# Optimization experiments

Hardware: AMD Instinct MI355X
Metric: run time of the kernel (lower is better)

The kernel has to match this reference:

```python
import jax, jax.numpy as jnp
import numpy as np

N = 50000       # nodes
E = 800000      # edges (before self-loops)
F_IN = 128      # in_channels
HID = 32        # hidden_channels per head
HEADS = 4
OUT = 16        # out_channels
NEG_SLOPE = 0.2 # PyG GATConv leaky_relu slope
EPS = 1e-16     # PyG softmax denominator eps
BN_EPS = 1e-5


def setup_inputs() -> dict:
    key = jax.random.key(0)
    ks = jax.random.split(key, 20)
    rn = lambda k, shp, s=0.1: (jax.random.normal(k, shp, jnp.float32) * s)
    x = jax.random.normal(ks[0], (N, F_IN), jnp.float32)
    edge_index = jax.random.randint(ks[1], (2, E), 0, N, dtype=jnp.int32)
    D0 = HEADS * HID  # 128
    return {
        "x": x, "edge_index": edge_index,
        # layer 0: GATConv(F_IN -> HID, heads=HEADS, concat=True)
        "W0": rn(ks[2], (F_IN, HEADS * HID)), "as0": rn(ks[3], (HEADS, HID)),
        "ad0": rn(ks[4], (HEADS, HID)), "b0": jnp.zeros((D0,), jnp.float32),
        "g0": jnp.ones((D0,), jnp.float32) + rn(ks[5], (D0,), 0.05),
        "be0": rn(ks[6], (D0,), 0.05),
        # layer 1: GATConv(D0 -> HID, heads=HEADS, concat=True)
        "W1": rn(ks[7], (D0, HEADS * HID)), "as1": rn(ks[8], (HEADS, HID)),
        "ad1": rn(ks[9], (HEADS, HID)), "b1": jnp.zeros((D0,), jnp.float32),
        "g1": jnp.ones((D0,), jnp.float32) + rn(ks[10], (D0,), 0.05),
        "be1": rn(ks[11], (D0,), 0.05),
        # layer 2: GATConv(D0 -> OUT, heads=1, concat=False)
        "W2": rn(ks[12], (D0, OUT)), "as2": rn(ks[13], (1, OUT)),
        "ad2": rn(ks[14], (1, OUT)), "b2": jnp.zeros((OUT,), jnp.float32),
    }


def _gat(x, src, dst, W, a_s, a_d, b, heads, ch, concat):
    n = x.shape[0]
    h = (x @ W).reshape(n, heads, ch)                       # [N,H,C]
    score_s = (h * a_s).sum(-1)                             # [N,H]
    score_d = (h * a_d).sum(-1)                             # [N,H]
    e = jax.nn.leaky_relu(score_s[src] + score_d[dst], NEG_SLOPE)  # [E,H]
    emax = jax.ops.segment_max(e, dst, num_segments=n)
    emax = jnp.where(jnp.isfinite(emax), emax, 0.0)
    p = jnp.exp(e - emax[dst])
    denom = jax.ops.segment_sum(p, dst, num_segments=n)
    alpha = p / (denom[dst] + EPS)                          # segment softmax over dst
    out = jax.ops.segment_sum(h[src] * alpha[:, :, None], dst, num_segments=n)
    out = out.reshape(n, heads * ch) if concat else out.mean(axis=1)
    return out + b


def _bn(x, g, be):
    m = x.mean(0)
    v = x.var(0)
    return (x - m) * jax.lax.rsqrt(v + BN_EPS) * g + be


def reference(x, edge_index, W0, as0, ad0, b0, g0, be0,
              W1, as1, ad1, b1, g1, be1, W2, as2, ad2, b2):
    n = x.shape[0]
    loop = jnp.arange(n, dtype=edge_index.dtype)
    src = jnp.concatenate([edge_index[0], loop])  # PyG add_self_loops
    dst = jnp.concatenate([edge_index[1], loop])
    h = _gat(x, src, dst, W0, as0, ad0, b0, HEADS, HID, True)
    h = jax.nn.elu(_bn(h, g0, be0))                 # dropout disabled (eval)
    h = _gat(h, src, dst, W1, as1, ad1, b1, HEADS, HID, True)
    h = jax.nn.elu(_bn(h, g1, be1))
    return _gat(h, src, dst, W2, as2, ad2, b2, 1, OUT, False)
```

## Files before the change

kernel.cpp:

```cpp
#include <hip/hip_runtime.h>
#include <hip/hip_bf16.h>
#include <math.h>

#define NEG_SLOPE 0.2f
#define EPS_SM 1e-16f
#define BN_EPS 1e-5f
#define RANK_BLOCKS 1024

typedef __attribute__((ext_vector_type(8))) short bf16x8;
typedef __attribute__((ext_vector_type(4))) float f32x4;

__device__ __forceinline__ float lrelu(float x) { return x > 0.f ? x : NEG_SLOPE * x; }
__device__ __forceinline__ ushort f2bf(float f) {
    uint u = __float_as_uint(f);
    return (ushort)((u + 0x7FFFu + ((u >> 16) & 1u)) >> 16);
}
__device__ __forceinline__ float bfl(uint u) { return __uint_as_float(u << 16); }
__device__ __forceinline__ float bfh(uint u) { return __uint_as_float(u & 0xFFFF0000u); }

__global__ void pack_w(const float* __restrict__ W0, const float* __restrict__ W1,
                       const float* __restrict__ W2, ushort* __restrict__ P0,
                       ushort* __restrict__ P1, ushort* __restrict__ P2) {
    int i = blockIdx.x * blockDim.x + threadIdx.x;
    const float* W;
    ushort* P;
    int NC, s;
    if (i < 16384) { W = W0; P = P0; NC = 128; s = i; }
    else if (i < 32768) { W = W1; P = P1; NC = 128; s = i - 16384; }
    else if (i < 34816) { W = W2; P = P2; NC = 16; s = i - 32768; }
    else return;
    int k = s / NC, col = s % NC;
    int CT = NC >> 4;
    int dst = (((k >> 5) * CT + (col >> 4)) << 9) +
              (((col & 15) | (((k >> 3) & 3) << 4)) << 3) + (k & 7);
    P[dst] = f2bf(W[s]);
}

template <int NC, int HEADS, bool XBN, bool RANKFUSE>
__global__ __launch_bounds__(256) void gemm_mfma(
    const void* __restrict__ Xv, const ushort* __restrict__ Wp, ushort* __restrict__ Hb,
    int n, const float* __restrict__ sumsP, const float* __restrict__ g,
    const float* __restrict__ be, const float* __restrict__ as_, const float* __restrict__ ad_,
    float* __restrict__ ss, float* __restrict__ sd,
    const int* __restrict__ dstE, int E, int* __restrict__ degP, ushort* __restrict__ rank) {
    int tid = threadIdx.x;
    if constexpr (RANKFUSE) {
        if ((int)blockIdx.x < RANK_BLOCKS) {
            const int T = RANK_BLOCKS * 256;
            int i = (int)blockIdx.x * 256 + tid;
            for (; i + 3 * T < E; i += 4 * T) {
                int d0 = dstE[i], d1 = dstE[i + T], d2 = dstE[i + 2 * T], d3 = dstE[i + 3 * T];
                ushort r0 = (ushort)atomicAdd(&degP[d0 << 4], 1);
                ushort r1 = (ushort)atomicAdd(&degP[d1 << 4], 1);
                ushort r2 = (ushort)atomicAdd(&degP[d2 << 4], 1);
                ushort r3 = (ushort)atomicAdd(&degP[d3 << 4], 1);
                rank[i] = r0;
                rank[i + T] = r1;
                rank[i + 2 * T] = r2;
                rank[i + 3 * T] = r3;
            }
            for (; i < E; i += T) rank[i] = (ushort)atomicAdd(&degP[dstE[i] << 4], 1);
            return;
        }
    }
    constexpr int CT = NC / 16;
    constexpr int FPH = NC / HEADS / 16;
    __shared__ __align__(16) ushort Xb[64 * 128];
    __shared__ float ssl[64 * HEADS], sdl[64 * HEADS];
    int bid = RANKFUSE ? ((int)blockIdx.x - RANK_BLOCKS) : (int)blockIdx.x;
    int row0 = bid * 64;
    if constexpr (!XBN) {
        const float* X = (const float*)Xv;
#pragma unroll
        for (int i = 0; i < 8; ++i) {
            int idx = tid + i * 256;
            int row = idx >> 5, q = idx & 31;
            int gr = row0 + row;
            float4 v = make_float4(0.f, 0.f, 0.f, 0.f);
            if (gr < n) v = ((const float4*)(X + (long)gr * 128))[q];
            ushort4 p = make_ushort4(f2bf(v.x), f2bf(v.y), f2bf(v.z), f2bf(v.w));
            int s = (q >> 1) ^ (row & 15);
            *(ushort4*)&Xb[row * 128 + s * 8 + (q & 1) * 4] = p;
        }
    } else {
        const ushort* X = (const ushort*)Xv;
        int c8 = (tid & 15) * 8;
        float inv_n = 1.f / (float)n;
        float bm[8], bs[8], bb[8];
#pragma unroll
        for (int j = 0; j < 8; ++j) {
            int ch = c8 + j;
            float m = sumsP[ch * 16] * inv_n;
            float vv = fmaxf(sumsP[(128 + ch) * 16] * inv_n - m * m, 0.f);
            bm[j] = m;
            bs[j] = rsqrtf(vv + BN_EPS) * g[ch];
            bb[j] = be[ch];
        }
#pragma unroll
        for (int i = 0; i < 4; ++i) {
            int idx = tid + i * 256;
            int row = idx >> 4, g8 = idx & 15;
            int gr = row0 + row;
            uint4 v = make_uint4(0, 0, 0, 0);
            if (gr < n) v = ((const uint4*)(X + (long)gr * 128))[g8];
            float a, b;
#define BNE(comp, j0)                                                  \
    a = bfl(comp); b = bfh(comp);                                      \
    a = (a - bm[j0]) * bs[j0] + bb[j0]; a = a > 0.f ? a : expm1f(a);   \
    b = (b - bm[j0 + 1]) * bs[j0 + 1] + bb[j0 + 1];                    \
    b = b > 0.f ? b : expm1f(b);                                       \
    comp = (uint)f2bf(a) | ((uint)f2bf(b) << 16);
            BNE(v.x, 0) BNE(v.y, 2) BNE(v.z, 4) BNE(v.w, 6)
#undef BNE
            int s = g8 ^ (row & 15);
            *(uint4*)&Xb[row * 128 + s * 8] = v;
        }
    }
    __syncthreads();
    int lane = tid & 63;
    int w = tid >> 6;
    int r0 = w * 16;
    int lrow = lane & 15, lhi = lane >> 4;
    f32x4 zero = {0.f, 0.f, 0.f, 0.f};
    f32x4 acc[CT];
#pragma unroll
    for (int f = 0; f < CT; ++f) acc[f] = zero;
    const ushort* xr = &Xb[(r0 + lrow) * 128];
#pragma unroll
    for (int ks = 0; ks < 4; ++ks) {
        int kg = ks * 4 + lhi;
        bf16x8 a = *(const bf16x8*)&xr[(kg ^ lrow) << 3];
#pragma unroll
        for (int f = 0; f < CT; ++f) {
            bf16x8 b = *(const bf16x8*)&Wp[((ks * CT + f) * 64 + lane) * 8];
            acc[f] = __builtin_amdgcn_mfma_f32_16x16x32_bf16(a, b, acc[f], 0, 0, 0);
        }
    }
    __syncthreads();
#pragma unroll
    for (int f = 0; f < CT; ++f)
#pragma unroll
        for (int j = 0; j < 4; ++j)
            Xb[(r0 + lhi * 4 + j) * NC + f * 16 + lrow] = f2bf(acc[f][j]);
    float asv[CT], adv[CT];
#pragma unroll
    for (int f = 0; f < CT; ++f) {
        asv[f] = as_[f * 16 + lrow];
        adv[f] = ad_[f * 16 + lrow];
    }
#pragma unroll
    for (int h = 0; h < HEADS; ++h) {
        float ps[4] = {}, pd[4] = {};
#pragma unroll
        for (int fi = 0; fi < FPH; ++fi) {
            int f = h * FPH + fi;
#pragma unroll
            for (int j = 0; j < 4; ++j) {
                ps[j] = fmaf(acc[f][j], asv[f], ps[j]);
                pd[j] = fmaf(acc[f][j], adv[f], pd[j]);
            }
        }
#pragma unroll
        for (int j = 0; j < 4; ++j) {
#pragma unroll
            for (int d = 1; d < 16; d <<= 1) {
                ps[j] += __shfl_xor(ps[j], d, 64);
                pd[j] += __shfl_xor(pd[j], d, 64);
            }
            if (lrow == 0) {
                ssl[(r0 + lhi * 4 + j) * HEADS + h] = ps[j];
                sdl[(r0 + lhi * 4 + j) * HEADS + h] = pd[j];
            }
        }
    }
    __syncthreads();
    constexpr int NU = 64 * NC / 8;
#pragma unroll
    for (int i = 0; i < (NU + 255) / 256; ++i) {
        int idx = tid + i * 256;
        if (idx < NU) {
            int row = idx / (NC / 8), c8i = idx % (NC / 8);
            int gr = row0 + row;
            if (gr < n) ((uint4*)&Hb[(long)gr * NC])[c8i] = ((const uint4*)Xb)[idx];
        }
    }
    if (tid < 64 * HEADS) {
        int row = tid / HEADS, hh = tid % HEADS;
        int gr = row0 + row;
        if (gr < n) {
            ss[(long)gr * HEADS + hh] = ssl[tid];
            sd[(long)gr * HEADS + hh] = sdl[tid];
        }
    }
}

__global__ void compact_deg(const int* __restrict__ degP, int* __restrict__ deg, int n) {
    int i = blockIdx.x * blockDim.x + threadIdx.x;
    if (i < n) deg[i] = degP[i << 4];
}

__global__ __launch_bounds__(1024) void scan_kernel(const int* __restrict__ deg,
                                                    int* __restrict__ offs, int n) {
    __shared__ int wsum[16];
    __shared__ int wpre[16];
    __shared__ int carry_s;
    int tid = threadIdx.x;
    int lane = tid & 63;
    int w = tid >> 6;
    if (tid == 0) carry_s = 0;
    __syncthreads();
    int nv = (n + 3) >> 2;
    for (int base = 0; base < nv; base += 1024) {
        int carry = carry_s;
        int gi = base + tid;
        int e0 = gi * 4;
        int4 v = make_int4(0, 0, 0, 0);
        if (e0 + 3 < n) {
            v = ((const int4*)deg)[gi];
        } else if (e0 < n) {
            v.x = deg[e0];
            if (e0 + 1 < n) v.y = deg[e0 + 1];
            if (e0 + 2 < n) v.z = deg[e0 + 2];
        }
        int tsum = v.x + v.y + v.z + v.w;
        int incl = tsum;
#pragma unroll
        for (int d = 1; d < 64; d <<= 1) {
            int t = __shfl_up(incl, d, 64);
            if (lane >= d) incl += t;
        }
        if (lane == 63) wsum[w] = incl;
        __syncthreads();
        if (w == 0 && lane < 16) {
            int s = wsum[lane];
#pragma unroll
            for (int d = 1; d < 16; d <<= 1) {
                int t = __shfl_up(s, d, 64);
                if (lane >= d) s += t;
            }
            wpre[lane] = s;
        }
        __syncthreads();
        int wbase = (w == 0) ? 0 : wpre[w - 1];
        int ex = carry + wbase + incl - tsum;
        if (e0 < n) {
            int4 o;
            o.x = ex;
            o.y = ex + v.x;
            o.z = o.y + v.y;
            o.w = o.z + v.z;
            if (e0 + 3 < n) {
                ((int4*)offs)[gi] = o;
            } else {
                offs[e0] = o.x;
                if (e0 + 1 < n) offs[e0 + 1] = o.y;
                if (e0 + 2 < n) offs[e0 + 2] = o.z;
            }
        }
        __syncthreads();
        if (tid == 1023) carry_s = carry + wpre[15];
        __syncthreads();
    }
    if (tid == 0) offs[n] = carry_s;
}

__global__ void scatter_kernel(const int* __restrict__ src, const int* __restrict__ dst,
                               const ushort* __restrict__ rank, const int* __restrict__ offs,
                               int E, int* __restrict__ srcs) {
    const int T = gridDim.x * blockDim.x;
    int i = blockIdx.x * blockDim.x + threadIdx.x;
    for (; i + 3 * T < E; i += 4 * T) {
        int d0 = dst[i], d1 = dst[i + T], d2 = dst[i + 2 * T], d3 = dst[i + 3 * T];
        int p0 = offs[d0] + (int)rank[i];
        int p1 = offs[d1] + (int)rank[i + T];
        int p2 = offs[d2] + (int)rank[i + 2 * T];
        int p3 = offs[d3] + (int)rank[i + 3 * T];
        srcs[p0] = src[i];
        srcs[p1] = src[i + T];
        srcs[p2] = src[i + 2 * T];
        srcs[p3] = src[i + 3 * T];
    }
    for (; i < E; i += T) srcs[offs[dst[i]] + (int)rank[i]] = src[i];
}

__global__ __launch_bounds__(256) void gat_gather4(
    const uint* __restrict__ hb, const float* __restrict__ ss, const float* __restrict__ sd,
    const int* __restrict__ offs, const int* __restrict__ srcs,
    const float* __restrict__ bias, ushort* __restrict__ outb, int n) {
    int wid = threadIdx.x >> 6;
    int lane = threadIdx.x & 63;
    int node = blockIdx.x * 4 + wid;
    if (node >= n) return;
    int off = offs[node];
    int dg = offs[node + 1] - off;
    int grp = lane >> 4;
    int ll = lane & 15;
    int hd = ll >> 2;
    float sdn = sd[node * 4 + hd];
    float es = lrelu(ss[node * 4 + hd] + sdn);
    const uint* hrow = hb + ll * 4;
    float acc[8] = {};
    float sm = 0.f;
    int i = grp;
    for (; i + 4 < dg; i += 8) {
        int s0 = srcs[off + i];
        int s1 = srcs[off + i + 4];
        float w0 = __expf(lrelu(ss[s0 * 4 + hd] + sdn));
        float w1 = __expf(lrelu(ss[s1 * 4 + hd] + sdn));
        uint4 h0 = *(const uint4*)(hrow + (long)s0 * 64);
        uint4 h1 = *(const uint4*)(hrow + (long)s1 * 64);
        sm += w0 + w1;
        acc[0] = fmaf(w0, bfl(h0.x), acc[0]); acc[0] = fmaf(w1, bfl(h1.x), acc[0]);
        acc[1] = fmaf(w0, bfh(h0.x), acc[1]); acc[1] = fmaf(w1, bfh(h1.x), acc[1]);
        acc[2] = fmaf(w0, bfl(h0.y), acc[2]); acc[2] = fmaf(w1, bfl(h1.y), acc[2]);
        acc[3] = fmaf(w0, bfh(h0.y), acc[3]); acc[3] = fmaf(w1, bfh(h1.y), acc[3]);
        acc[4] = fmaf(w0, bfl(h0.z), acc[4]); acc[4] = fmaf(w1, bfl(h1.z), acc[4]);
        acc[5] = fmaf(w0, bfh(h0.z), acc[5]); acc[5] = fmaf(w1, bfh(h1.z), acc[5]);
        acc[6] = fmaf(w0, bfl(h0.w), acc[6]); acc[6] = fmaf(w1, bfl(h1.w), acc[6]);
        acc[7] = fmaf(w0, bfh(h0.w), acc[7]); acc[7] = fmaf(w1, bfh(h1.w), acc[7]);
    }
    for (; i < dg; i += 4) {
        int s = srcs[off + i];
        float w = __expf(lrelu(ss[s * 4 + hd] + sdn));
        sm += w;
        uint4 hv = *(const uint4*)(hrow + (long)s * 64);
        acc[0] = fmaf(w, bfl(hv.x), acc[0]);
        acc[1] = fmaf(w, bfh(hv.x), acc[1]);
        acc[2] = fmaf(w, bfl(hv.y), acc[2]);
        acc[3] = fmaf(w, bfh(hv.y), acc[3]);
        acc[4] = fmaf(w, bfl(hv.z), acc[4]);
        acc[5] = fmaf(w, bfh(hv.z), acc[5]);
        acc[6] = fmaf(w, bfl(hv.w), acc[6]);
        acc[7] = fmaf(w, bfh(hv.w), acc[7]);
    }
#pragma unroll
    for (int j = 0; j < 8; ++j) {
        acc[j] += __shfl_xor(acc[j], 16, 64);
        acc[j] += __shfl_xor(acc[j], 32, 64);
    }
    sm += __shfl_xor(sm, 16, 64);
    sm += __shfl_xor(sm, 32, 64);
    float wS = __expf(es);
    sm += wS;
    uint4 hvS = *(const uint4*)(hrow + (long)node * 64);
    acc[0] = fmaf(wS, bfl(hvS.x), acc[0]);
    acc[1] = fmaf(wS, bfh(hvS.x), acc[1]);
    acc[2] = fmaf(wS, bfl(hvS.y), acc[2]);
    acc[3] = fmaf(wS, bfh(hvS.y), acc[3]);
    acc[4] = fmaf(wS, bfl(hvS.z), acc[4]);
    acc[5] = fmaf(wS, bfh(hvS.z), acc[5]);
    acc[6] = fmaf(wS, bfl(hvS.w), acc[6]);
    acc[7] = fmaf(wS, bfh(hvS.w), acc[7]);
    float inv = 1.f / (sm + EPS_SM);
    if (grp == 0) {
        float4 bA = *(const float4*)&bias[ll * 8];
        float4 bB = *(const float4*)&bias[ll * 8 + 4];
        uint4 p;
        p.x = (uint)f2bf(acc[0] * inv + bA.x) | ((uint)f2bf(acc[1] * inv + bA.y) << 16);
        p.y = (uint)f2bf(acc[2] * inv + bA.z) | ((uint)f2bf(acc[3] * inv + bA.w) << 16);
        p.z = (uint)f2bf(acc[4] * inv + bB.x) | ((uint)f2bf(acc[5] * inv + bB.y) << 16);
        p.w = (uint)f2bf(acc[6] * inv + bB.z) | ((uint)f2bf(acc[7] * inv + bB.w) << 16);
        *(uint4*)&outb[(long)node * 128 + ll * 8] = p;
    }
}

__global__ __launch_bounds__(256) void gat_gather1(
    const uint* __restrict__ hb2, const float* __restrict__ ss, const float* __restrict__ sd,
    const int* __restrict__ offs, const int* __restrict__ srcs,
    const float* __restrict__ bias, float* __restrict__ out, int n) {
    int wid = threadIdx.x >> 6;
    int lane = threadIdx.x & 63;
    int node = blockIdx.x * 4 + wid;
    if (node >= n) return;
    int off = offs[node];
    int dg = offs[node + 1] - off;
    int grp = lane >> 3;
    int ll = lane & 7;
    float sdn = sd[node];
    float es = lrelu(ss[node] + sdn);
    float a0 = 0.f, a1 = 0.f, sm = 0.f;
    int i = grp;
    for (; i + 8 < dg; i += 16) {
        int s0 = srcs[off + i];
        int s1 = srcs[off + i + 8];
        float w0 = __expf(lrelu(ss[s0] + sdn));
        float w1 = __expf(lrelu(ss[s1] + sdn));
        uint h0 = hb2[s0 * 8 + ll];
        uint h1 = hb2[s1 * 8 + ll];
        sm += w0 + w1;
        a0 = fmaf(w0, bfl(h0), a0); a0 = fmaf(w1, bfl(h1), a0);
        a1 = fmaf(w0, bfh(h0), a1); a1 = fmaf(w1, bfh(h1), a1);
    }
    for (; i < dg; i += 8) {
        int s = srcs[off + i];
        float w = __expf(lrelu(ss[s] + sdn));
        sm += w;
        uint hv = hb2[s * 8 + ll];
        a0 = fmaf(w, bfl(hv), a0);
        a1 = fmaf(w, bfh(hv), a1);
    }
#pragma unroll
    for (int d = 8; d <= 32; d <<= 1) {
        a0 += __shfl_xor(a0, d, 64);
        a1 += __shfl_xor(a1, d, 64);
        sm += __shfl_xor(sm, d, 64);
    }
    float wS = __expf(es);
    sm += wS;
    uint hvS = hb2[node * 8 + ll];
    a0 = fmaf(wS, bfl(hvS), a0);
    a1 = fmaf(wS, bfh(hvS), a1);
    float inv = 1.f / (sm + EPS_SM);
    if (grp == 0) {
        float2 o = make_float2(a0 * inv + bias[ll * 2], a1 * inv + bias[ll * 2 + 1]);
        *(float2*)&out[(long)node * 16 + ll * 2] = o;
    }
}

__global__ __launch_bounds__(256) void bn_stats_bf16(const uint4* __restrict__ X4,
                                                     float* __restrict__ sumsP, int n) {
    __shared__ float red[4096];
    int tid = threadIdx.x;
    float s[8] = {}, s2[8] = {};
    long tot = (long)n * 16;
    long T = (long)gridDim.x * 256;
    for (long i = (long)blockIdx.x * 256 + tid; i < tot; i += T) {
        uint4 v = X4[i];
        float f;
        f = bfl(v.x); s[0] += f; s2[0] = fmaf(f, f, s2[0]);
        f = bfh(v.x); s[1] += f; s2[1] = fmaf(f, f, s2[1]);
        f = bfl(v.y); s[2] += f; s2[2] = fmaf(f, f, s2[2]);
        f = bfh(v.y); s[3] += f; s2[3] = fmaf(f, f, s2[3]);
        f = bfl(v.z); s[4] += f; s2[4] = fmaf(f, f, s2[4]);
        f = bfh(v.z); s[5] += f; s2[5] = fmaf(f, f, s2[5]);
        f = bfl(v.w); s[6] += f; s2[6] = fmaf(f, f, s2[6]);
        f = bfh(v.w); s[7] += f; s2[7] = fmaf(f, f, s2[7]);
    }
#pragma unroll
    for (int j = 0; j < 8; ++j) {
        red[j * 256 + tid] = s[j];
        red[(8 + j) * 256 + tid] = s2[j];
    }
    __syncthreads();
    int ch = tid & 127, st = tid >> 7;
    int base = (st * 8 + (ch & 7)) * 256 + (ch >> 3);
    float a = 0.f;
#pragma unroll
    for (int rep = 0; rep < 16; ++rep) a += red[base + rep * 16];
    atomicAdd(&sumsP[tid * 16], a);
}

extern "C" void kernel_launch(void* const* d_in, const int* in_sizes, int n_in,
                              void* d_out, int out_size, void* d_ws, size_t ws_size,
                              hipStream_t stream) {
    const float* x = (const float*)d_in[0];
    const int* ei = (const int*)d_in[1];
    const float* W0 = (const float*)d_in[2];
    const float* as0 = (const float*)d_in[3];
    const float* ad0 = (const float*)d_in[4];
    const float* b0 = (const float*)d_in[5];
    const float* g0 = (const float*)d_in[6];
    const float* be0 = (const float*)d_in[7];
    const float* W1 = (const float*)d_in[8];
    const float* as1 = (const float*)d_in[9];
    const float* ad1 = (const float*)d_in[10];
    const float* b1 = (const float*)d_in[11];
    const float* g1 = (const float*)d_in[12];
    const float* be1 = (const float*)d_in[13];
    const float* W2 = (const float*)d_in[14];
    const float* as2 = (const float*)d_in[15];
    const float* ad2 = (const float*)d_in[16];
    const float* b2 = (const float*)d_in[17];

    int n = in_sizes[0] / 128;
    int E = in_sizes[1] / 2;
    const int* srcA = ei;
    const int* dstA = ei + E;

    char* base = (char*)d_ws;
    auto alloc = [&](size_t bytes) {
        char* p = base;
        base += (bytes + 255) & ~(size_t)255;
        return p;
    };
    ushort* hb = (ushort*)alloc((size_t)n * 128 * 2);
    ushort* actb = (ushort*)alloc((size_t)n * 128 * 2);
    ushort* h2b = (ushort*)alloc((size_t)n * 16 * 2);
    float* ssb = (float*)alloc((size_t)n * 4 * 4);
    float* sdb = (float*)alloc((size_t)n * 4 * 4);
    float* sumsP0 = (float*)alloc(4096 * 4);
    float* sumsP1 = (float*)alloc(4096 * 4);
    int* degP = (int*)alloc((size_t)n * 64);
    int* deg = (int*)alloc((size_t)n * 4);
    int* offs = (int*)alloc(((size_t)n + 1) * 4);
    ushort* rank = (ushort*)alloc((size_t)E * 2);
    int* srcs = (int*)alloc((size_t)E * 4);
    ushort* Wp0 = (ushort*)alloc(16384 * 2);
    ushort* Wp1 = (ushort*)alloc(16384 * 2);
    ushort* Wp2 = (ushort*)alloc(2048 * 2);

    float* out = (float*)d_out;

    hipMemsetAsync(degP, 0, (size_t)n * 64, stream);
    hipMemsetAsync(sumsP0, 0, 4096 * 4 * 2, stream);

    pack_w<<<136, 256, 0, stream>>>(W0, W1, W2, Wp0, Wp1, Wp2);

    int gGemm = (n + 63) / 64;
    int gWave = (n + 3) / 4;
    int gNode = (n + 255) / 256;

    gemm_mfma<128, 4, false, true><<<RANK_BLOCKS + gGemm, 256, 0, stream>>>(
        x, Wp0, hb, n, nullptr, g0, be0, as0, ad0, ssb, sdb, dstA, E, degP, rank);
    compact_deg<<<gNode, 256, 0, stream>>>(degP, deg, n);
    scan_kernel<<<1, 1024, 0, stream>>>(deg, offs, n);
    scatter_kernel<<<2048, 256, 0, stream>>>(srcA, dstA, rank, offs, E, srcs);

    gat_gather4<<<gWave, 256, 0, stream>>>((const uint*)hb, ssb, sdb, offs, srcs, b0, actb, n);
    bn_stats_bf16<<<256, 256, 0, stream>>>((const uint4*)actb, sumsP0, n);

    gemm_mfma<128, 4, true, false><<<gGemm, 256, 0, stream>>>(
        actb, Wp1, hb, n, sumsP0, g0, be0, as1, ad1, ssb, sdb, nullptr, 0, nullptr, nullptr);
    gat_gather4<<<gWave, 256, 0, stream>>>((const uint*)hb, ssb, sdb, offs, srcs, b1, actb, n);
    bn_stats_bf16<<<256, 256, 0, stream>>>((const uint4*)actb, sumsP1, n);

    gemm_mfma<16, 1, true, false><<<gGemm, 256, 0, stream>>>(
        actb, Wp2, h2b, n, sumsP1, g1, be1, as2, ad2, ssb, sdb, nullptr, 0, nullptr, nullptr);
    gat_gather1<<<gWave, 256, 0, stream>>>((const uint*)h2b, ssb, sdb, offs, srcs, b2, out, n);
}
```

Baseline: 243.0 us.

## Build CSR via two-level bucket sort with LDS atomics instead of global atomics

Replaces the global-atomic degree counting, per-edge rank array, compaction and scatter with a two-pass bucket sort. Edges are first histogrammed and scattered into 256-node buckets, with counters held in shared memory per chunk. A per-bucket kernel then builds the fine offsets and source lists using LDS atomics. This removes the contended, padded global atomics and the degP memset, but it adds launches, an extra packed-edge pass, and drops the overlap with the first GEMM. The packed format assumes node ids fit in 24 bits.

```diff
diff --git a/kernel.cpp b/kernel.cpp
--- a/kernel.cpp
+++ b/kernel.cpp
@@ -5,7 +5,7 @@
 #define NEG_SLOPE 0.2f
 #define EPS_SM 1e-16f
 #define BN_EPS 1e-5f
-#define RANK_BLOCKS 1024
+#define CHUNKS 256
 
 typedef __attribute__((ext_vector_type(8))) short bf16x8;
 typedef __attribute__((ext_vector_type(4))) float f32x4;
@@ -36,39 +36,87 @@
     P[dst] = f2bf(W[s]);
 }
 
-template <int NC, int HEADS, bool XBN, bool RANKFUSE>
+
+__global__ __launch_bounds__(256) void bucket_count(const int* __restrict__ dst, int E,
+                                                    int* __restrict__ hist, int nbuck) {
+    __shared__ int h[256];
+    int blk = blockIdx.x, tid = threadIdx.x;
+    h[tid] = 0;
+    __syncthreads();
+    int e0 = (int)(((long)E * blk) >> 8);
+    int e1 = (int)(((long)E * (blk + 1)) >> 8);
+    for (int i = e0 + tid; i < e1; i += 256) atomicAdd(&h[dst[i] >> 8], 1);
+    __syncthreads();
+    if (tid < nbuck) hist[tid * CHUNKS + blk] = h[tid];
+}
+
+__global__ __launch_bounds__(256) void bucket_scatter(const int* __restrict__ src,
+                                                      const int* __restrict__ dst, int E,
+                                                      const int* __restrict__ base,
+                                                      uint* __restrict__ bpack, int nbuck) {
+    __shared__ int cur[256];
+    int blk = blockIdx.x, tid = threadIdx.x;
+    if (tid < nbuck) cur[tid] = base[tid * CHUNKS + blk];
+    __syncthreads();
+    int e0 = (int)(((long)E * blk) >> 8);
+    int e1 = (int)(((long)E * (blk + 1)) >> 8);
+    for (int i = e0 + tid; i < e1; i += 256) {
+        int d = dst[i];
+        int p = atomicAdd(&cur[d >> 8], 1);
+        bpack[p] = ((uint)src[i] << 8) | (uint)(d & 255);
+    }
+}
+
+__global__ __launch_bounds__(256) void fine_csr(const uint* __restrict__ bpack,
+                                                const int* __restrict__ base, int E, int n,
+                                                int* __restrict__ offs, int* __restrict__ srcs,
+                                                int nbuck) {
+    __shared__ int cnt[256];
+    __shared__ int wsum[4];
+    int bk = blockIdx.x, tid = threadIdx.x;
+    int ebase = base[bk * CHUNKS];
+    int eend = base[(bk + 1) * CHUNKS];
+    cnt[tid] = 0;
+    __syncthreads();
+    for (int i = ebase + tid; i < eend; i += 256) atomicAdd(&cnt[bpack[i] & 255], 1);
+    __syncthreads();
+    int lane = tid & 63, w = tid >> 6;
+    int v = cnt[tid];
+    int incl = v;
+#pragma unroll
+    for (int d = 1; d < 64; d <<= 1) {
+        int t = __shfl_up(incl, d, 64);
+        if (lane >= d) incl += t;
+    }
+    if (lane == 63) wsum[w] = incl;
+    __syncthreads();
+    int wbase = 0;
+    for (int j = 0; j < w; ++j) wbase += wsum[j];
+    int excl = wbase + incl - v;
+    int node = bk * 256 + tid;
+    if (node < n) offs[node] = ebase + excl;
+    cnt[tid] = ebase + excl;
+    __syncthreads();
+    for (int i = ebase + tid; i < eend; i += 256) {
+        uint pk = bpack[i];
+        int p = atomicAdd(&cnt[pk & 255], 1);
+        srcs[p] = (int)(pk >> 8);
+    }
+    if (bk == nbuck - 1 && tid == 0) offs[n] = E;
+}
+
+template <int NC, int HEADS, bool XBN>
 __global__ __launch_bounds__(256) void gemm_mfma(
     const void* __restrict__ Xv, const ushort* __restrict__ Wp, ushort* __restrict__ Hb,
     int n, const float* __restrict__ sumsP, const float* __restrict__ g,
     const float* __restrict__ be, const float* __restrict__ as_, const float* __restrict__ ad_,
-    float* __restrict__ ss, float* __restrict__ sd,
-    const int* __restrict__ dstE, int E, int* __restrict__ degP, ushort* __restrict__ rank) {
+    float* __restrict__ ss, float* __restrict__ sd) {
     int tid = threadIdx.x;
-    if constexpr (RANKFUSE) {
-        if ((int)blockIdx.x < RANK_BLOCKS) {
-            const int T = RANK_BLOCKS * 256;
-            int i = (int)blockIdx.x * 256 + tid;
-            for (; i + 3 * T < E; i += 4 * T) {
-                int d0 = dstE[i], d1 = dstE[i + T], d2 = dstE[i + 2 * T], d3 = dstE[i + 3 * T];
-                ushort r0 = (ushort)atomicAdd(&degP[d0 << 4], 1);
-                ushort r1 = (ushort)atomicAdd(&degP[d1 << 4], 1);
-                ushort r2 = (ushort)atomicAdd(&degP[d2 << 4], 1);
-                ushort r3 = (ushort)atomicAdd(&degP[d3 << 4], 1);
-                rank[i] = r0;
-                rank[i + T] = r1;
-                rank[i + 2 * T] = r2;
-                rank[i + 3 * T] = r3;
-            }
-            for (; i < E; i += T) rank[i] = (ushort)atomicAdd(&degP[dstE[i] << 4], 1);
-            return;
-        }
-    }
     constexpr int CT = NC / 16;
     constexpr int FPH = NC / HEADS / 16;
     __shared__ __align__(16) ushort Xb[64 * 128];
     __shared__ float ssl[64 * HEADS], sdl[64 * HEADS];
-    int bid = RANKFUSE ? ((int)blockIdx.x - RANK_BLOCKS) : (int)blockIdx.x;
-    int row0 = bid * 64;
+    int row0 = (int)blockIdx.x * 64;
     if constexpr (!XBN) {
         const float* X = (const float*)Xv;
 #pragma unroll
@@ -194,11 +242,6 @@
     }
 }
 
-__global__ void compact_deg(const int* __restrict__ degP, int* __restrict__ deg, int n) {
-    int i = blockIdx.x * blockDim.x + threadIdx.x;
-    if (i < n) deg[i] = degP[i << 4];
-}
-
 __global__ __launch_bounds__(1024) void scan_kernel(const int* __restrict__ deg,
                                                     int* __restrict__ offs, int n) {
     __shared__ int wsum[16];
@@ -262,25 +305,6 @@
         __syncthreads();
     }
     if (tid == 0) offs[n] = carry_s;
-}
-
-__global__ void scatter_kernel(const int* __restrict__ src, const int* __restrict__ dst,
-                               const ushort* __restrict__ rank, const int* __restrict__ offs,
-                               int E, int* __restrict__ srcs) {
-    const int T = gridDim.x * blockDim.x;
-    int i = blockIdx.x * blockDim.x + threadIdx.x;
-    for (; i + 3 * T < E; i += 4 * T) {
-        int d0 = dst[i], d1 = dst[i + T], d2 = dst[i + 2 * T], d3 = dst[i + 3 * T];
-        int p0 = offs[d0] + (int)rank[i];
-        int p1 = offs[d1] + (int)rank[i + T];
-        int p2 = offs[d2] + (int)rank[i + 2 * T];
-        int p3 = offs[d3] + (int)rank[i + 3 * T];
-        srcs[p0] = src[i];
-        srcs[p1] = src[i + T];
-        srcs[p2] = src[i + 2 * T];
-        srcs[p3] = src[i + 3 * T];
-    }
-    for (; i < E; i += T) srcs[offs[dst[i]] + (int)rank[i]] = src[i];
 }
 
 __global__ __launch_bounds__(256) void gat_gather4(
@@ -476,6 +500,7 @@
     int E = in_sizes[1] / 2;
     const int* srcA = ei;
     const int* dstA = ei + E;
+    int nbuck = (n + 255) >> 8;
 
     char* base = (char*)d_ws;
     auto alloc = [&](size_t bytes) {
@@ -490,10 +515,10 @@
     float* sdb = (float*)alloc((size_t)n * 4 * 4);
     float* sumsP0 = (float*)alloc(4096 * 4);
     float* sumsP1 = (float*)alloc(4096 * 4);
-    int* degP = (int*)alloc((size_t)n * 64);
-    int* deg = (int*)alloc((size_t)n * 4);
+    int* hist = (int*)alloc(((size_t)nbuck * CHUNKS + 1) * 4);
+    int* bbase = (int*)alloc(((size_t)nbuck * CHUNKS + 1) * 4);
+    uint* bpack = (uint*)alloc((size_t)E * 4);
     int* offs = (int*)alloc(((size_t)n + 1) * 4);
-    ushort* rank = (ushort*)alloc((size_t)E * 2);
     int* srcs = (int*)alloc((size_t)E * 4);
     ushort* Wp0 = (ushort*)alloc(16384 * 2);
     ushort* Wp1 = (ushort*)alloc(16384 * 2);
@@ -501,30 +526,30 @@
 
     float* out = (float*)d_out;
 
-    hipMemsetAsync(degP, 0, (size_t)n * 64, stream);
     hipMemsetAsync(sumsP0, 0, 4096 * 4 * 2, stream);
 
     pack_w<<<136, 256, 0, stream>>>(W0, W1, W2, Wp0, Wp1, Wp2);
 
     int gGemm = (n + 63) / 64;
     int gWave = (n + 3) / 4;
-    int gNode = (n + 255) / 256;
-
-    gemm_mfma<128, 4, false, true><<<RANK_BLOCKS + gGemm, 256, 0, stream>>>(
-        x, Wp0, hb, n, nullptr, g0, be0, as0, ad0, ssb, sdb, dstA, E, degP, rank);
-    compact_deg<<<gNode, 256, 0, stream>>>(degP, deg, n);
-    scan_kernel<<<1, 1024, 0, stream>>>(deg, offs, n);
-    scatter_kernel<<<2048, 256, 0, stream>>>(srcA, dstA, rank, offs, E, srcs);
+
+    gemm_mfma<128, 4, false><<<gGemm, 256, 0, stream>>>(
+        x, Wp0, hb, n, nullptr, g0, be0, as0, ad0, ssb, sdb);
+
+    bucket_count<<<CHUNKS, 256, 0, stream>>>(dstA, E, hist, nbuck);
+    scan_kernel<<<1, 1024, 0, stream>>>(hist, bbase, nbuck * CHUNKS);
+    bucket_scatter<<<CHUNKS, 256, 0, stream>>>(srcA, dstA, E, bbase, bpack, nbuck);
+    fine_csr<<<nbuck, 256, 0, stream>>>(bpack, bbase, E, n, offs, srcs, nbuck);
 
     gat_gather4<<<gWave, 256, 0, stream>>>((const uint*)hb, ssb, sdb, offs, srcs, b0, actb, n);
     bn_stats_bf16<<<256, 256, 0, stream>>>((const uint4*)actb, sumsP0, n);
 
-    gemm_mfma<128, 4, true, false><<<gGemm, 256, 0, stream>>>(
-        actb, Wp1, hb, n, sumsP0, g0, be0, as1, ad1, ssb, sdb, nullptr, 0, nullptr, nullptr);
+    gemm_mfma<128, 4, true><<<gGemm, 256, 0, stream>>>(
+        actb, Wp1, hb, n, sumsP0, g0, be0, as1, ad1, ssb, sdb);
     gat_gather4<<<gWave, 256, 0, stream>>>((const uint*)hb, ssb, sdb, offs, srcs, b1, actb, n);
     bn_stats_bf16<<<256, 256, 0, stream>>>((const uint4*)actb, sumsP1, n);
 
-    gemm_mfma<16, 1, true, false><<<gGemm, 256, 0, stream>>>(
-        actb, Wp2, h2b, n, sumsP1, g1, be1, as2, ad2, ssb, sdb, nullptr, 0, nullptr, nullptr);
+    gemm_mfma<16, 1, true><<<gGemm, 256, 0, stream>>>(
+        actb, Wp2, h2b, n, sumsP1, g1, be1, as2, ad2, ssb, sdb);
     gat_gather1<<<gWave, 256, 0, stream>>>((const uint*)h2b, ssb, sdb, offs, srcs, b2, out, n);
 }
```

Result: faster. 223.1 us (-8.2%).
